# Performance work log

Measured on AMD Instinct MI355X. Metric: run time of the kernel, lower is better.

Reference implementation:

```python
import jax, jax.numpy as jnp
import numpy as np

B, S, D, H = 4, 2048, 512, 8
HD = D // H  # head_dim = 64


def setup_inputs() -> dict:
    key = jax.random.key(0)
    ks = jax.random.split(key, 16)
    sd = 1.0 / np.sqrt(D)
    def lin(ka, kb):
        W = jax.random.uniform(ka, (D, D), jnp.float32, -sd, sd)
        b = jax.random.uniform(kb, (D,), jnp.float32, -sd, sd)
        return W, b
    Wq, bq = lin(ks[0], ks[1])
    Wk, bk = lin(ks[2], ks[3])
    Wv, bv = lin(ks[4], ks[5])
    Wo, bo = lin(ks[6], ks[7])
    Ws, bs = lin(ks[8], ks[9])
    Wsh, bsh = lin(ks[10], ks[11])
    mod1_feat = jax.random.normal(ks[12], (B, S, D), jnp.float32)
    mod2_feat = jax.random.normal(ks[13], (B, S, D), jnp.float32)
    return {"mod1_feat": mod1_feat, "mod2_feat": mod2_feat,
            "Wq": Wq, "bq": bq, "Wk": Wk, "bk": bk, "Wv": Wv, "bv": bv,
            "Wo": Wo, "bo": bo, "Ws": Ws, "bs": bs, "Wsh": Wsh, "bsh": bsh}


def _heads(x):
    # [B, S, D] -> [B, H, S, HD]
    b, s, _ = x.shape
    return x.reshape(b, s, H, HD).transpose(0, 2, 1, 3)


def reference(mod1_feat, mod2_feat, Wq, bq, Wk, bk, Wv, bv, Wo, bo, Ws, bs, Wsh, bsh):
    Q = _heads(mod1_feat @ Wq + bq)
    K = _heads(mod2_feat @ Wk + bk)
    V = _heads(mod2_feat @ Wv + bv)
    scale = _heads(mod2_feat @ Ws + bs)
    shift = _heads(mod2_feat @ Wsh + bsh)
    K = K * scale + shift
    V = V * scale + shift
    scores = jnp.einsum('bhqd,bhkd->bhqk', Q, K) / jnp.sqrt(jnp.float32(HD))
    attn = jax.nn.softmax(scores, axis=-1)
    out = jnp.einsum('bhqk,bhkd->bhqd', attn, V)  # [B, H, S, HD]
    out = out.transpose(0, 2, 1, 3).reshape(mod1_feat.shape[0], -1, H * HD)
    return out @ Wo + bo
```

## Files before the change

kernel.cpp:

```cpp
#include <hip/hip_runtime.h>
#include <hip/hip_bf16.h>
#include <cstdint>
#include <cstddef>

typedef __bf16 bf16_t;
typedef __bf16 bf16x8 __attribute__((ext_vector_type(8)));
typedef __bf16 bf16x4 __attribute__((ext_vector_type(4)));
typedef float f32x4 __attribute__((ext_vector_type(4)));

#define DEVINL static __device__ __forceinline__

constexpr int B_ = 4, S_ = 2048, D_ = 512, H_ = 8, HD_ = 64;
constexpr int M_ = B_ * S_;
constexpr int NIN = 14;

DEVINL bf16x8 load8g(const bf16_t* p) { return *reinterpret_cast<const bf16x8*>(p); }

DEVINL int swcol(int col, int row) {
  return (col & ~63) | ((((col >> 3) ^ row) & 7) << 3) | (col & 7);
}

DEVINL int pK(int row) { return (row & 3) | (((row >> 3) & 1) << 2); }
DEVINL int swcolK(int col, int row) {
  return (col & ~63) | ((((col >> 3) ^ pK(row)) & 7) << 3) | (col & 7);
}

DEVINL void gl2lds(const bf16_t* g, bf16_t* l) {
  __builtin_amdgcn_global_load_lds(
      (const __attribute__((address_space(1))) void*)g,
      (__attribute__((address_space(3))) void*)l, 16, 0, 0);
}

DEVINL void stage16(bf16_t* dst, const void* src, size_t off, bool f32) {
  if (f32) {
    const float* p = (const float*)src + off;
    bf16x8 v0, v1;
#pragma unroll
    for (int j = 0; j < 8; ++j) { v0[j] = (bf16_t)p[j]; v1[j] = (bf16_t)p[8 + j]; }
    *reinterpret_cast<bf16x8*>(dst)     = v0;
    *reinterpret_cast<bf16x8*>(dst + 8) = v1;
  } else {
    const bf16_t* p = (const bf16_t*)src + off;
    *reinterpret_cast<bf16x8*>(dst)     = load8g(p);
    *reinterpret_cast<bf16x8*>(dst + 8) = load8g(p + 8);
  }
}

DEVINL float readf(const void* p, size_t i, bool f32) {
  return f32 ? ((const float*)p)[i] : (float)((const bf16_t*)p)[i];
}

DEVINL bool block_detect(const uint16_t* p, int n, int* dsum) {
  const int t = threadIdx.x;
  int cnt = 0;
  for (int i = t; i < n; i += 256) cnt += (((p[i] >> 7) & 0xFF) >= 200);
#pragma unroll
  for (int off = 32; off > 0; off >>= 1) cnt += __shfl_down(cnt, off, 64);
  if ((t & 63) == 0) dsum[t >> 6] = cnt;
  __syncthreads();
  const int tot = dsum[0] + dsum[1] + dsum[2] + dsum[3];
  __syncthreads();
  return tot > 16;
}

struct PrepArgs {
  const void* csrc[2]; bf16_t* cdst[2];
  const void* wsrc[6]; bf16_t* wdst[6];
  const uint16_t* dp[NIN]; int dn[NIN];
  int* flags;
};

__global__ __launch_bounds__(256) void prep_kernel(PrepArgs a) {
  __shared__ bf16_t tile[64][80];
  __shared__ int dsum[4];
  const int bid = blockIdx.x;
  const int t = threadIdx.x;
  if (bid < 2048) {
    const int z = bid >> 10;
    const bool f32 = block_detect((const uint16_t*)a.csrc[z], 2048, dsum);
    const size_t i = ((size_t)(bid & 1023) * 256 + t) * 16;
    const int row = (int)(i >> 9);
    const int col = (int)(i & 511);
    bf16_t* dst = a.cdst[z] + (size_t)row * 512;
    bf16x8 v0, v1;
    if (f32) {
      const float* p = (const float*)a.csrc[z] + i;
      const f32x4 f0 = *reinterpret_cast<const f32x4*>(p);
      const f32x4 f1 = *reinterpret_cast<const f32x4*>(p + 4);
      const f32x4 f2 = *reinterpret_cast<const f32x4*>(p + 8);
      const f32x4 f3 = *reinterpret_cast<const f32x4*>(p + 12);
#pragma unroll
      for (int j = 0; j < 4; ++j) {
        v0[j] = (bf16_t)f0[j]; v0[4 + j] = (bf16_t)f1[j];
        v1[j] = (bf16_t)f2[j]; v1[4 + j] = (bf16_t)f3[j];
      }
    } else {
      const bf16_t* p = (const bf16_t*)a.csrc[z] + i;
      v0 = load8g(p); v1 = load8g(p + 8);
    }
    *reinterpret_cast<bf16x8*>(dst + swcol(col, row))     = v0;
    *reinterpret_cast<bf16x8*>(dst + swcol(col + 8, row)) = v1;
  } else if (bid < 2432) {
    const int rem = bid - 2048;
    const int w = rem >> 6;
    const int r6 = rem & 63;
    const int k0 = (r6 & 7) * 64, n0 = (r6 >> 3) * 64;
    const void* src = a.wsrc[w];
    const bool f32 = block_detect((const uint16_t*)src, 2048, dsum);
    bf16_t* dst = a.wdst[w];
    const int r = t >> 2, c0 = (t & 3) * 16;
    stage16(&tile[r][c0], src, (size_t)(k0 + r) * 512 + n0 + c0, f32);
    __syncthreads();
    const int orow = n0 + r;
    bf16_t* o = dst + (size_t)orow * 512;
#pragma unroll
    for (int half = 0; half < 2; ++half) {
      bf16x8 ov;
#pragma unroll
      for (int j = 0; j < 8; ++j) ov[j] = tile[c0 + half * 8 + j][r];
      *reinterpret_cast<bf16x8*>(o + swcol(k0 + c0 + half * 8, orow)) = ov;
    }
  } else {
    const int z = bid - 2432;
    const bool f32 = block_detect(a.dp[z], a.dn[z], dsum);
    if (t == 0) a.flags[z] = f32 ? 1 : 0;
  }
}

struct GemmBatch {
  const bf16_t* A[3];
  const bf16_t* Bt[3];
  const void* bias[3]; int bIdx[3];
  void* C[3];          int cIdx[3];
  const int* flags;
};

__global__ __launch_bounds__(512) void gemm_bt_kernel(GemmBatch args) {
  constexpr int K = 512, N = 512;
  __shared__ bf16_t As[3][128][64];
  __shared__ bf16_t Bs[3][64][64];
  const int z = blockIdx.z;
  const bf16_t* Ag  = args.A[z];
  const bf16_t* Btg = args.Bt[z];
  const int m0 = blockIdx.x * 128, n0 = blockIdx.y * 64;
  const int t = threadIdx.x, lane = t & 63, wave = t >> 6;
  const int l16 = lane & 15, quad = lane >> 4;
  const int wm = wave * 16;
  const int lr = lane >> 3, lc = (lane & 7) * 8;

  auto stage = [&](int slot, int k0) {
#pragma unroll
    for (int s = 0; s < 2; ++s) {
      const int r = wm + s * 8;
      gl2lds(Ag + (size_t)(m0 + r + lr) * K + k0 + lc, &As[slot][r][0]);
    }
    gl2lds(Btg + (size_t)(n0 + wave * 8 + lr) * K + k0 + lc, &Bs[slot][wave * 8][0]);
  };

  f32x4 acc[4] = {};

  stage(0, 0);
  stage(1, 64);

  constexpr int NT = K / 64;
  int cur = 0;
  for (int kt = 0; kt < NT - 1; ++kt) {
    asm volatile("s_waitcnt vmcnt(3)\n\ts_barrier" ::: "memory");
    __builtin_amdgcn_sched_barrier(0);
    if (kt + 2 < NT) {
      const int slot2 = cur == 0 ? 2 : cur - 1;
      stage(slot2, (kt + 2) * 64);
    }
#pragma unroll
    for (int ks = 0; ks < 2; ++ks) {
      const int sw = swcol(ks * 32 + quad * 8, l16);
      bf16x8 af = *reinterpret_cast<const bf16x8*>(&As[cur][wm + l16][sw]);
      bf16x8 bfr[4];
#pragma unroll
      for (int j = 0; j < 4; ++j)
        bfr[j] = *reinterpret_cast<const bf16x8*>(&Bs[cur][j * 16 + l16][sw]);
#pragma unroll
      for (int j = 0; j < 4; ++j)
        acc[j] = __builtin_amdgcn_mfma_f32_16x16x32_bf16(af, bfr[j], acc[j], 0, 0, 0);
    }
    cur = (cur == 2) ? 0 : cur + 1;
  }
  asm volatile("s_waitcnt vmcnt(0)\n\ts_barrier" ::: "memory");
  __builtin_amdgcn_sched_barrier(0);
#pragma unroll
  for (int ks = 0; ks < 2; ++ks) {
    const int sw = swcol(ks * 32 + quad * 8, l16);
    bf16x8 af = *reinterpret_cast<const bf16x8*>(&As[cur][wm + l16][sw]);
    bf16x8 bfr[4];
#pragma unroll
    for (int j = 0; j < 4; ++j)
      bfr[j] = *reinterpret_cast<const bf16x8*>(&Bs[cur][j * 16 + l16][sw]);
#pragma unroll
    for (int j = 0; j < 4; ++j)
      acc[j] = __builtin_amdgcn_mfma_f32_16x16x32_bf16(af, bfr[j], acc[j], 0, 0, 0);
  }

  const void* biag = args.bias[z];
  void* Cg         = args.C[z];
  const bool bf32 = args.bIdx[z] >= 0 && args.flags[args.bIdx[z]];
  const bool cf32 = args.cIdx[z] >= 0 && args.flags[args.cIdx[z]];
#pragma unroll
  for (int j = 0; j < 4; ++j) {
    const int col = n0 + j * 16 + l16;
    const float bv = readf(biag, col, bf32);
    const int rowb = m0 + wm + quad * 4;
#pragma unroll
    for (int r = 0; r < 4; ++r) {
      const size_t idx = (size_t)(rowb + r) * N + col;
      const float v = acc[j][r] + bv;
      if (cf32) ((float*)Cg)[idx] = v;
      else      ((bf16_t*)Cg)[idx] = (bf16_t)v;
    }
  }
}

struct KsvArgs {
  const bf16_t* A;
  const bf16_t* Bt[4];
  const void* bias[4]; int bIdx[4];
  bf16_t* Kmod;
  bf16_t* VtT;
  const int* flags;
};

__global__ __launch_bounds__(1024) void ksv_kernel(KsvArgs args) {
  constexpr int K = 512;
  __shared__ bf16_t As[3][128][64];
  __shared__ bf16_t Bs[3][4][64][64];
  const int m0 = blockIdx.x * 128, n0 = blockIdx.y * 64;
  const int t = threadIdx.x, lane = t & 63, wave = t >> 6;
  const int l16 = lane & 15, quad = lane >> 4;
  const int wm = (wave >> 2) * 32;
  const int wn = (wave & 3) * 16;
  const int lr = lane >> 3, lc = (lane & 7) * 8;

  auto stage = [&](int slot, int k0) {
    gl2lds(args.A + (size_t)(m0 + wave * 8 + lr) * K + k0 + lc, &As[slot][wave * 8][0]);
    const int mat = wave >> 2;
    const int rb = (wave & 3) * 16;
#pragma unroll
    for (int s = 0; s < 2; ++s) {
      const int r = rb + s * 8;
      gl2lds(args.Bt[mat] + (size_t)(n0 + r + lr) * K + k0 + lc, &Bs[slot][mat][r][0]);
    }
  };

  f32x4 acc[4][2] = {};

  stage(0, 0);
  stage(1, 64);

  constexpr int NT = K / 64;
  int cur = 0;
  for (int kt = 0; kt < NT - 1; ++kt) {
    asm volatile("s_waitcnt vmcnt(3)\n\ts_barrier" ::: "memory");
    __builtin_amdgcn_sched_barrier(0);
    if (kt + 2 < NT) {
      const int slot2 = cur == 0 ? 2 : cur - 1;
      stage(slot2, (kt + 2) * 64);
    }
#pragma unroll
    for (int ks = 0; ks < 2; ++ks) {
      const int sw = swcol(ks * 32 + quad * 8, l16);
      bf16x8 af[2], bfr[4];
#pragma unroll
      for (int mi = 0; mi < 2; ++mi)
        af[mi] = *reinterpret_cast<const bf16x8*>(&As[cur][wm + mi * 16 + l16][sw]);
#pragma unroll
      for (int mat = 0; mat < 4; ++mat)
        bfr[mat] = *reinterpret_cast<const bf16x8*>(&Bs[cur][mat][wn + l16][sw]);
#pragma unroll
      for (int mat = 0; mat < 4; ++mat)
#pragma unroll
        for (int mi = 0; mi < 2; ++mi)
          acc[mat][mi] = __builtin_amdgcn_mfma_f32_16x16x32_bf16(af[mi], bfr[mat], acc[mat][mi], 0, 0, 0);
    }
    cur = (cur == 2) ? 0 : cur + 1;
  }
  asm volatile("s_waitcnt vmcnt(0)\n\ts_barrier" ::: "memory");
  __builtin_amdgcn_sched_barrier(0);
#pragma unroll
  for (int ks = 0; ks < 2; ++ks) {
    const int sw = swcol(ks * 32 + quad * 8, l16);
    bf16x8 af[2], bfr[4];
#pragma unroll
    for (int mi = 0; mi < 2; ++mi)
      af[mi] = *reinterpret_cast<const bf16x8*>(&As[cur][wm + mi * 16 + l16][sw]);
#pragma unroll
    for (int mat = 0; mat < 4; ++mat)
      bfr[mat] = *reinterpret_cast<const bf16x8*>(&Bs[cur][mat][wn + l16][sw]);
#pragma unroll
    for (int mat = 0; mat < 4; ++mat)
#pragma unroll
      for (int mi = 0; mi < 2; ++mi)
        acc[mat][mi] = __builtin_amdgcn_mfma_f32_16x16x32_bf16(af[mi], bfr[mat], acc[mat][mi], 0, 0, 0);
  }

  const int col = n0 + wn + l16;
  const float bk  = readf(args.bias[0], col, args.bIdx[0] >= 0 && args.flags[args.bIdx[0]]);
  const float bv  = readf(args.bias[1], col, args.bIdx[1] >= 0 && args.flags[args.bIdx[1]]);
  const float bs  = readf(args.bias[2], col, args.bIdx[2] >= 0 && args.flags[args.bIdx[2]]);
  const float bsh = readf(args.bias[3], col, args.bIdx[3] >= 0 && args.flags[args.bIdx[3]]);
  const int hh = col >> 6, dd = col & 63;
#pragma unroll
  for (int mi = 0; mi < 2; ++mi) {
    const int rowb = m0 + wm + mi * 16 + quad * 4;
    bf16x4 vpack;
#pragma unroll
    for (int r = 0; r < 4; ++r) {
      const int row = rowb + r;
      const float s  = acc[2][mi][r] + bs;
      const float sh = acc[3][mi][r] + bsh;
      const float kk = fmaf(acc[0][mi][r] + bk, s, sh);
      const float vv = fmaf(acc[1][mi][r] + bv, s, sh);
      args.Kmod[(size_t)row * 512 + swcolK(col, row)] = (bf16_t)kk;
      vpack[r] = (bf16_t)vv;
    }
    const int bb = rowb >> 11;
    const int ss = rowb & 2047;
    *reinterpret_cast<bf16x4*>(
        args.VtT + (((size_t)(bb * H_ + hh)) * HD_ + dd) * S_ + swcol(ss, dd)) = vpack;
  }
}

__global__ __launch_bounds__(512) void attn_kernel(const bf16_t* M1, const bf16_t* Wq,
                                                   const void* bq, const int* flags,
                                                   const bf16_t* Kb, const bf16_t* Vt,
                                                   bf16_t* O) {
  __shared__ bf16_t Ks[3][64][64];
  __shared__ bf16_t Vs[3][64][64];
  __shared__ bf16_t Xs[3][64][64];
  const int i = blockIdx.x;
  const int xcd = i & 7, g = i >> 3;
  const int slice = xcd * 4 + (g & 3);
  const int qt = g >> 2;
  const int b = slice >> 3, h = slice & 7;
  const int t = threadIdx.x, wave = t >> 6, lane = t & 63;
  const int l16 = lane & 15, quad = lane >> 4;
  const int q0 = qt * 128 + wave * 16;
  const int lr = lane >> 3, lc = (lane & 7) * 8;

  constexpr float CE = 0.18033688011112042f;

  const size_t q0g = (size_t)b * S_ + qt * 128;

  auto qstage = [&](int set, int k0) {
#pragma unroll
    for (int s = 0; s < 2; ++s) {
      const int r = wave * 16 + s * 8;
      bf16_t* dst = (wave < 4) ? &Ks[set][r][0] : &Vs[set][r - 64][0];
      gl2lds(M1 + (q0g + r + lr) * D_ + k0 + lc, dst);
    }
    gl2lds(Wq + (size_t)(h * HD_ + wave * 8 + lr) * D_ + k0 + lc, &Xs[set][wave * 8][0]);
  };

  f32x4 qacc[4] = {};
  const bf16_t* brow = (wave < 4) ? &Ks[0][wave * 16][0] : &Vs[0][wave * 16 - 64][0];
  const int setstride = 64 * 64;

  auto qcompute = [&](int set) {
    const bf16_t* bbase = brow + set * setstride;
#pragma unroll
    for (int ks = 0; ks < 2; ++ks) {
      const int sw = swcol(ks * 32 + quad * 8, l16);
      bf16x8 bf = *reinterpret_cast<const bf16x8*>(bbase + l16 * 64 + sw);
      bf16x8 af[4];
#pragma unroll
      for (int j = 0; j < 4; ++j)
        af[j] = *reinterpret_cast<const bf16x8*>(&Xs[set][j * 16 + l16][sw]);
#pragma unroll
      for (int j = 0; j < 4; ++j)
        qacc[j] = __builtin_amdgcn_mfma_f32_16x16x32_bf16(af[j], bf, qacc[j], 0, 0, 0);
    }
  };

  qstage(0, 0);
  qstage(1, 64);
  {
    constexpr int QNT = D_ / 64;
    int cur = 0;
    for (int kt = 0; kt < QNT - 1; ++kt) {
      asm volatile("s_waitcnt vmcnt(3)\n\ts_barrier" ::: "memory");
      __builtin_amdgcn_sched_barrier(0);
      if (kt + 2 < QNT) {
        const int slot2 = cur == 0 ? 2 : cur - 1;
        qstage(slot2, (kt + 2) * 64);
      }
      qcompute(cur);
      cur = (cur == 2) ? 0 : cur + 1;
    }
    asm volatile("s_waitcnt vmcnt(0)\n\ts_barrier" ::: "memory");
    __builtin_amdgcn_sched_barrier(0);
    qcompute(cur);
  }
  const bool qbf32 = flags[3] != 0;
  __syncthreads();
  bf16_t* qls = &Xs[0][0][0];
#pragma unroll
  for (int j = 0; j < 4; ++j) {
    bf16x4 pk;
#pragma unroll
    for (int r = 0; r < 4; ++r) {
      const int d = j * 16 + quad * 4 + r;
      pk[r] = (bf16_t)((qacc[j][r] + readf(bq, h * HD_ + d, qbf32)) * CE);
    }
    *reinterpret_cast<bf16x4*>(&qls[wave * 1024 + l16 * 64 + swcol(j * 16 + quad * 4, l16)]) = pk;
  }
  __syncthreads();
  bf16x8 qf[2];
#pragma unroll
  for (int dc = 0; dc < 2; ++dc)
    qf[dc] = *reinterpret_cast<const bf16x8*>(&qls[wave * 1024 + l16 * 64 + swcol(dc * 32 + quad * 8, l16)]);

  bf16x8 ones;
#pragma unroll
  for (int j = 0; j < 8; ++j) ones[j] = (bf16_t)1.0f;

  f32x4 oacc[4] = {};
  f32x4 lacc = {};

  const size_t kbase = (size_t)b * S_ * D_ + h * HD_;
  const size_t vbase = ((size_t)(b * H_ + h)) * HD_ * S_;

  const int rbase = ((l16 >> 2) << 3) | (l16 & 3);
  int koff[2][4];
#pragma unroll
  for (int j = 0; j < 4; ++j) {
    const int rho = rbase + (j >> 1) * 32 + (j & 1) * 4;
#pragma unroll
    for (int dc = 0; dc < 2; ++dc)
      koff[dc][j] = rho * 64 + swcolK(dc * 32 + quad * 8, rho);
  }
  const int voff[2] = { swcol(quad * 8, l16), swcol(32 + quad * 8, l16) };

  auto stage = [&](int slot, int k0) {
    const int r = wave * 8;
    gl2lds(Kb + kbase + (size_t)(k0 + r + lr) * D_ + lc, &Ks[slot][r][0]);
    gl2lds(Vt + vbase + (size_t)(r + lr) * S_ + k0 + lc, &Vs[slot][r][0]);
  };

  auto compute = [&](int cur) {
    f32x4 sacc[4] = {};
    const bf16_t* ksbase = &Ks[cur][0][0];
#pragma unroll
    for (int dc = 0; dc < 2; ++dc) {
      bf16x8 kf[4];
#pragma unroll
      for (int j = 0; j < 4; ++j)
        kf[j] = *reinterpret_cast<const bf16x8*>(ksbase + koff[dc][j]);
#pragma unroll
      for (int j = 0; j < 4; ++j)
        sacc[j] = __builtin_amdgcn_mfma_f32_16x16x32_bf16(kf[j], qf[dc], sacc[j], 0, 0, 0);
    }
#pragma unroll
    for (int kc = 0; kc < 2; ++kc) {
      bf16x8 vf[4];
#pragma unroll
      for (int dj = 0; dj < 4; ++dj)
        vf[dj] = *reinterpret_cast<const bf16x8*>(&Vs[cur][dj * 16 + l16][voff[kc]]);
      bf16x8 bp;
#pragma unroll
      for (int r = 0; r < 4; ++r) {
        bp[r]     = (bf16_t)__builtin_amdgcn_exp2f(fminf(sacc[kc * 2][r],     57.5f));
        bp[4 + r] = (bf16_t)__builtin_amdgcn_exp2f(fminf(sacc[kc * 2 + 1][r], 57.5f));
      }
#pragma unroll
      for (int dj = 0; dj < 4; ++dj)
        oacc[dj] = __builtin_amdgcn_mfma_f32_16x16x32_bf16(vf[dj], bp, oacc[dj], 0, 0, 0);
      lacc = __builtin_amdgcn_mfma_f32_16x16x32_bf16(ones, bp, lacc, 0, 0, 0);
    }
  };

  asm volatile("s_waitcnt vmcnt(0)" ::: "memory");
  stage(0, 0);
  stage(1, 64);

  constexpr int NT = S_ / 64;
  int cur = 0;
  for (int kt = 0; kt < NT - 1; ++kt) {
    asm volatile("s_waitcnt vmcnt(2)\n\ts_barrier" ::: "memory");
    __builtin_amdgcn_sched_barrier(0);
    if (kt + 2 < NT) {
      const int slot2 = cur == 0 ? 2 : cur - 1;
      stage(slot2, (kt + 2) * 64);
    }
    compute(cur);
    cur = (cur == 2) ? 0 : cur + 1;
  }
  asm volatile("s_waitcnt vmcnt(0)\n\ts_barrier" ::: "memory");
  __builtin_amdgcn_sched_barrier(0);
  compute(cur);

  {
    const float linv = 1.0f / fmaxf(lacc[0], 1e-30f);
    const int q = q0 + l16;
    const size_t orow = ((size_t)b * S_ + q) * D_ + h * HD_;
#pragma unroll
    for (int dj = 0; dj < 4; ++dj) {
      bf16x4 pack;
#pragma unroll
      for (int r = 0; r < 4; ++r) pack[r] = (bf16_t)(oacc[dj][r] * linv);
      *reinterpret_cast<bf16x4*>(&O[orow + swcol(dj * 16 + quad * 4, q)]) = pack;
    }
  }
}

extern "C" void kernel_launch(void* const* d_in, const int* in_sizes, int n_in,
                              void* d_out, int out_size, void* d_ws, size_t ws_size,
                              hipStream_t stream) {
  (void)n_in; (void)out_size; (void)ws_size;

  char* ws = (char*)d_ws;
  auto alloc = [&](size_t bytes) -> char* {
    char* p = ws; ws += (bytes + 255) & ~(size_t)255; return p;
  };
  int* flags = (int*)alloc(64 * sizeof(int));
  const size_t wbytes = (size_t)512 * 512 * sizeof(bf16_t);
  const size_t fbytes = (size_t)M_ * D_ * sizeof(bf16_t);
  bf16_t* wt    = (bf16_t*)alloc(6 * wbytes);
  bf16_t* m1b   = (bf16_t*)alloc(fbytes);
  bf16_t* m2b   = (bf16_t*)alloc(fbytes);
  bf16_t* vtb   = (bf16_t*)alloc(fbytes);
  bf16_t* atmp  = (bf16_t*)alloc(fbytes);
  bf16_t* kmod  = (bf16_t*)alloc(fbytes);
  bf16_t* attn_b = atmp;

  bf16_t* wtq  = wt + 0 * 512 * 512;
  bf16_t* wtk  = wt + 1 * 512 * 512;
  bf16_t* wtv  = wt + 2 * 512 * 512;
  bf16_t* wts  = wt + 3 * 512 * 512;
  bf16_t* wtsh = wt + 4 * 512 * 512;
  bf16_t* wto  = wt + 5 * 512 * 512;

  PrepArgs pa;
  pa.csrc[0] = d_in[0]; pa.cdst[0] = m1b;
  pa.csrc[1] = d_in[1]; pa.cdst[1] = m2b;
  const int widx[6] = {2, 4, 6, 10, 12, 8};
  bf16_t* wdst[6] = {wtq, wtk, wtv, wts, wtsh, wto};
  for (int i = 0; i < 6; ++i) { pa.wsrc[i] = d_in[widx[i]]; pa.wdst[i] = wdst[i]; }
  for (int i = 0; i < NIN; ++i) {
    pa.dp[i] = (const uint16_t*)d_in[i];
    pa.dn[i] = in_sizes[i] < 2048 ? in_sizes[i] : 2048;
  }
  pa.flags = flags;
  hipLaunchKernelGGL(prep_kernel, dim3(2048 + 384 + 14), dim3(256), 0, stream, pa);

  KsvArgs kv;
  kv.A = m2b;
  kv.Bt[0] = wtk; kv.Bt[1] = wtv; kv.Bt[2] = wts; kv.Bt[3] = wtsh;
  kv.bias[0] = d_in[5];  kv.bIdx[0] = 5;
  kv.bias[1] = d_in[7];  kv.bIdx[1] = 7;
  kv.bias[2] = d_in[11]; kv.bIdx[2] = 11;
  kv.bias[3] = d_in[13]; kv.bIdx[3] = 13;
  kv.Kmod = kmod; kv.VtT = vtb;
  kv.flags = flags;
  hipLaunchKernelGGL(ksv_kernel, dim3(M_ / 128, 8), dim3(1024), 0, stream, kv);

  hipLaunchKernelGGL(attn_kernel, dim3(512), dim3(512), 0, stream,
                     m1b, wtq, d_in[3], flags, kmod, vtb, attn_b);

  GemmBatch g2;
  for (int i = 0; i < 3; ++i) {
    g2.A[i] = attn_b;
    g2.Bt[i] = wto;
    g2.bias[i] = d_in[9]; g2.bIdx[i] = 9;
    g2.C[i] = d_out; g2.cIdx[i] = 0;
  }
  g2.flags = flags;
  hipLaunchKernelGGL(gemm_bt_kernel, dim3(M_ / 128, 8, 1), dim3(512), 0, stream, g2);
}
```

Before: 191.6 us.

## Split K/V projection kernel over grid z, recompute scale, stream scale weights from registers

```diff
diff --git a/kernel.cpp b/kernel.cpp
--- a/kernel.cpp
+++ b/kernel.cpp
@@ -228,103 +228,108 @@
   const int* flags;
 };
 
-__global__ __launch_bounds__(1024) void ksv_kernel(KsvArgs args) {
+__global__ __launch_bounds__(512) void ksv_kernel(KsvArgs args) {
   constexpr int K = 512;
-  __shared__ bf16_t As[3][128][64];
-  __shared__ bf16_t Bs[3][4][64][64];
+  __shared__ bf16_t As[2][128][64];
+  __shared__ bf16_t Bs[2][2][64][64];
+  const int z = blockIdx.z;
+  const bf16_t* Ag    = args.A;
+  const bf16_t* Bmain = args.Bt[z];
+  const bf16_t* Bsh   = args.Bt[3];
+  const bf16_t* Bsc   = args.Bt[2];
   const int m0 = blockIdx.x * 128, n0 = blockIdx.y * 64;
   const int t = threadIdx.x, lane = t & 63, wave = t >> 6;
   const int l16 = lane & 15, quad = lane >> 4;
-  const int wm = (wave >> 2) * 32;
+  const int wm = (wave >> 2) * 64;
   const int wn = (wave & 3) * 16;
   const int lr = lane >> 3, lc = (lane & 7) * 8;
 
-  auto stage = [&](int slot, int k0) {
-    gl2lds(args.A + (size_t)(m0 + wave * 8 + lr) * K + k0 + lc, &As[slot][wave * 8][0]);
-    const int mat = wave >> 2;
-    const int rb = (wave & 3) * 16;
+  const int srow = n0 + wn + l16;
+  const bf16_t* sp = Bsc + (size_t)srow * 512;
+
+  auto stage = [&](int buf, int k0) {
 #pragma unroll
     for (int s = 0; s < 2; ++s) {
-      const int r = rb + s * 8;
-      gl2lds(args.Bt[mat] + (size_t)(n0 + r + lr) * K + k0 + lc, &Bs[slot][mat][r][0]);
-    }
-  };
-
-  f32x4 acc[4][2] = {};
+      const int r = wave * 16 + s * 8;
+      gl2lds(Ag + (size_t)(m0 + r + lr) * K + k0 + lc, &As[buf][r][0]);
+    }
+    const int mat = wave & 1;
+    const int rb = (wave >> 1) * 16;
+    const bf16_t* bp = mat ? Bsh : Bmain;
+#pragma unroll
+    for (int s = 0; s < 2; ++s)
+      gl2lds(bp + (size_t)(n0 + rb + s * 8 + lr) * K + k0 + lc, &Bs[buf][mat][rb + s * 8][0]);
+  };
+
+  f32x4 acc[3][4] = {};
+  bf16x8 sfr[2];
 
   stage(0, 0);
-  stage(1, 64);
+  sfr[0] = load8g(sp + swcol(quad * 8, srow));
+  sfr[1] = load8g(sp + swcol(32 + quad * 8, srow));
 
   constexpr int NT = K / 64;
-  int cur = 0;
-  for (int kt = 0; kt < NT - 1; ++kt) {
-    asm volatile("s_waitcnt vmcnt(3)\n\ts_barrier" ::: "memory");
-    __builtin_amdgcn_sched_barrier(0);
-    if (kt + 2 < NT) {
-      const int slot2 = cur == 0 ? 2 : cur - 1;
-      stage(slot2, (kt + 2) * 64);
+  for (int kt = 0; kt < NT; ++kt) {
+    const int cur = kt & 1;
+    __syncthreads();
+    bf16x8 snx0, snx1;
+    if (kt + 1 < NT) {
+      stage(1 - cur, (kt + 1) * 64);
+      snx0 = load8g(sp + swcol((kt + 1) * 64 + quad * 8, srow));
+      snx1 = load8g(sp + swcol((kt + 1) * 64 + 32 + quad * 8, srow));
     }
 #pragma unroll
     for (int ks = 0; ks < 2; ++ks) {
       const int sw = swcol(ks * 32 + quad * 8, l16);
-      bf16x8 af[2], bfr[4];
-#pragma unroll
-      for (int mi = 0; mi < 2; ++mi)
+      bf16x8 af[4];
+#pragma unroll
+      for (int mi = 0; mi < 4; ++mi)
         af[mi] = *reinterpret_cast<const bf16x8*>(&As[cur][wm + mi * 16 + l16][sw]);
-#pragma unroll
-      for (int mat = 0; mat < 4; ++mat)
-        bfr[mat] = *reinterpret_cast<const bf16x8*>(&Bs[cur][mat][wn + l16][sw]);
-#pragma unroll
-      for (int mat = 0; mat < 4; ++mat)
-#pragma unroll
-        for (int mi = 0; mi < 2; ++mi)
-          acc[mat][mi] = __builtin_amdgcn_mfma_f32_16x16x32_bf16(af[mi], bfr[mat], acc[mat][mi], 0, 0, 0);
-    }
-    cur = (cur == 2) ? 0 : cur + 1;
-  }
-  asm volatile("s_waitcnt vmcnt(0)\n\ts_barrier" ::: "memory");
-  __builtin_amdgcn_sched_barrier(0);
-#pragma unroll
-  for (int ks = 0; ks < 2; ++ks) {
-    const int sw = swcol(ks * 32 + quad * 8, l16);
-    bf16x8 af[2], bfr[4];
-#pragma unroll
-    for (int mi = 0; mi < 2; ++mi)
-      af[mi] = *reinterpret_cast<const bf16x8*>(&As[cur][wm + mi * 16 + l16][sw]);
-#pragma unroll
-    for (int mat = 0; mat < 4; ++mat)
-      bfr[mat] = *reinterpret_cast<const bf16x8*>(&Bs[cur][mat][wn + l16][sw]);
-#pragma unroll
-    for (int mat = 0; mat < 4; ++mat)
-#pragma unroll
-      for (int mi = 0; mi < 2; ++mi)
-        acc[mat][mi] = __builtin_amdgcn_mfma_f32_16x16x32_bf16(af[mi], bfr[mat], acc[mat][mi], 0, 0, 0);
+      const bf16x8 b0 = *reinterpret_cast<const bf16x8*>(&Bs[cur][0][wn + l16][sw]);
+      const bf16x8 b1 = *reinterpret_cast<const bf16x8*>(&Bs[cur][1][wn + l16][sw]);
+#pragma unroll
+      for (int mi = 0; mi < 4; ++mi)
+        acc[0][mi] = __builtin_amdgcn_mfma_f32_16x16x32_bf16(af[mi], b0, acc[0][mi], 0, 0, 0);
+#pragma unroll
+      for (int mi = 0; mi < 4; ++mi)
+        acc[1][mi] = __builtin_amdgcn_mfma_f32_16x16x32_bf16(af[mi], sfr[ks], acc[1][mi], 0, 0, 0);
+#pragma unroll
+      for (int mi = 0; mi < 4; ++mi)
+        acc[2][mi] = __builtin_amdgcn_mfma_f32_16x16x32_bf16(af[mi], b1, acc[2][mi], 0, 0, 0);
+    }
+    if (kt + 1 < NT) { sfr[0] = snx0; sfr[1] = snx1; }
   }
 
   const int col = n0 + wn + l16;
-  const float bk  = readf(args.bias[0], col, args.bIdx[0] >= 0 && args.flags[args.bIdx[0]]);
-  const float bv  = readf(args.bias[1], col, args.bIdx[1] >= 0 && args.flags[args.bIdx[1]]);
+  const float bm  = readf(args.bias[z], col, args.bIdx[z] >= 0 && args.flags[args.bIdx[z]]);
   const float bs  = readf(args.bias[2], col, args.bIdx[2] >= 0 && args.flags[args.bIdx[2]]);
   const float bsh = readf(args.bias[3], col, args.bIdx[3] >= 0 && args.flags[args.bIdx[3]]);
   const int hh = col >> 6, dd = col & 63;
 #pragma unroll
-  for (int mi = 0; mi < 2; ++mi) {
+  for (int mi = 0; mi < 4; ++mi) {
     const int rowb = m0 + wm + mi * 16 + quad * 4;
-    bf16x4 vpack;
-#pragma unroll
-    for (int r = 0; r < 4; ++r) {
-      const int row = rowb + r;
-      const float s  = acc[2][mi][r] + bs;
-      const float sh = acc[3][mi][r] + bsh;
-      const float kk = fmaf(acc[0][mi][r] + bk, s, sh);
-      const float vv = fmaf(acc[1][mi][r] + bv, s, sh);
-      args.Kmod[(size_t)row * 512 + swcolK(col, row)] = (bf16_t)kk;
-      vpack[r] = (bf16_t)vv;
-    }
-    const int bb = rowb >> 11;
-    const int ss = rowb & 2047;
-    *reinterpret_cast<bf16x4*>(
-        args.VtT + (((size_t)(bb * H_ + hh)) * HD_ + dd) * S_ + swcol(ss, dd)) = vpack;
+    if (z == 0) {
+#pragma unroll
+      for (int r = 0; r < 4; ++r) {
+        const int row = rowb + r;
+        const float s  = acc[1][mi][r] + bs;
+        const float sh = acc[2][mi][r] + bsh;
+        args.Kmod[(size_t)row * 512 + swcolK(col, row)] =
+            (bf16_t)fmaf(acc[0][mi][r] + bm, s, sh);
+      }
+    } else {
+      bf16x4 vpack;
+#pragma unroll
+      for (int r = 0; r < 4; ++r) {
+        const float s  = acc[1][mi][r] + bs;
+        const float sh = acc[2][mi][r] + bsh;
+        vpack[r] = (bf16_t)fmaf(acc[0][mi][r] + bm, s, sh);
+      }
+      const int bb = rowb >> 11;
+      const int ss = rowb & 2047;
+      *reinterpret_cast<bf16x4*>(
+          args.VtT + (((size_t)(bb * H_ + hh)) * HD_ + dd) * S_ + swcol(ss, dd)) = vpack;
+    }
   }
 }
 
@@ -559,7 +564,7 @@
   kv.bias[3] = d_in[13]; kv.bIdx[3] = 13;
   kv.Kmod = kmod; kv.VtT = vtb;
   kv.flags = flags;
-  hipLaunchKernelGGL(ksv_kernel, dim3(M_ / 128, 8), dim3(1024), 0, stream, kv);
+  hipLaunchKernelGGL(ksv_kernel, dim3(M_ / 128, 8, 2), dim3(512), 0, stream, kv);
 
   hipLaunchKernelGGL(attn_kernel, dim3(512), dim3(512), 0, stream,
                      m1b, wtq, d_in[3], flags, kmod, vtb, attn_b);
```

Result: slower. 197.1 us (+2.9%).
